# Performance work log

Measured on AMD Instinct MI355X. Metric: run time of the kernel, lower is better.

The kernel has to match this reference:

```python
import jax, jax.numpy as jnp
import numpy as np

N = 100000      # nodes
E = 1600000     # edges
IN = 128        # input features
HID = 16        # hidden per head
HEADS = 4
OUT = 40        # output classes per head
NEG = 0.2       # leaky_relu slope (DGL default)
EPS = 1e-5      # BN eps


def setup_inputs() -> dict:
    key = jax.random.key(0)
    ks = jax.random.split(key, 24)
    rn = lambda k, s, sc=0.1: jax.random.normal(k, s, jnp.float32) * sc
    return {
        "feat": rn(ks[0], (N, IN), 1.0),
        "src": jax.random.randint(ks[1], (E,), 0, N, jnp.int32),
        "dst": jax.random.randint(ks[2], (E,), 0, N, jnp.int32),
        "W0": rn(ks[3], (IN, HEADS * HID)),
        "al0": rn(ks[4], (HEADS, HID)),
        "ar0": rn(ks[5], (HEADS, HID)),
        "b0": jnp.zeros((HEADS * HID,), jnp.float32),
        "resW0": rn(ks[6], (IN, HEADS * HID)),
        "gamma0": jnp.ones((HEADS * HID,), jnp.float32),
        "beta0": jnp.zeros((HEADS * HID,), jnp.float32),
        "W1": rn(ks[7], (HEADS * HID, HEADS * HID)),
        "al1": rn(ks[8], (HEADS, HID)),
        "ar1": rn(ks[9], (HEADS, HID)),
        "b1": jnp.zeros((HEADS * HID,), jnp.float32),
        "gamma1": jnp.ones((HEADS * HID,), jnp.float32),
        "beta1": jnp.zeros((HEADS * HID,), jnp.float32),
        "W2": rn(ks[10], (HEADS * HID, HEADS * OUT)),
        "al2": rn(ks[11], (HEADS, OUT)),
        "ar2": rn(ks[12], (HEADS, OUT)),
        "b2": jnp.zeros((HEADS * OUT,), jnp.float32),
        "resW2": rn(ks[13], (HEADS * HID, HEADS * OUT)),
    }


def gat_conv(h, src, dst, W, al, ar, b, res):
    # h: [N, F_in]; res: [N, H*D] (res_fc output or identity)
    n = h.shape[0]
    H, D = al.shape
    feat = (h @ W).reshape(n, H, D)                 # [N,H,D]
    el = jnp.einsum('nhd,hd->nh', feat, al)         # [N,H]
    er = jnp.einsum('nhd,hd->nh', feat, ar)
    e = jax.nn.leaky_relu(el[src] + er[dst], NEG)   # [E,H]
    # edge softmax over destination nodes
    m = jax.ops.segment_max(e, dst, num_segments=n)
    ee = jnp.exp(e - m[dst])
    denom = jax.ops.segment_sum(ee, dst, num_segments=n)
    alpha = ee / jnp.maximum(denom[dst], 1e-16)     # [E,H]
    rst = jax.ops.segment_sum(alpha[:, :, None] * feat[src], dst, num_segments=n)
    rst = rst + res.reshape(n, H, D) + b.reshape(1, H, D)
    return rst.reshape(n, H * D)


def batch_norm(h, gamma, beta):
    mu = jnp.mean(h, axis=0)
    var = jnp.var(h, axis=0)
    return (h - mu) * jax.lax.rsqrt(var + EPS) * gamma + beta


def reference(feat, src, dst, W0, al0, ar0, b0, resW0, gamma0, beta0,
              W1, al1, ar1, b1, gamma1, beta1, W2, al2, ar2, b2, resW2):
    # layer 0: res_fc is a Linear (128 != 64); outer residual skipped (dims differ)
    h = gat_conv(feat, src, dst, W0, al0, ar0, b0, feat @ resW0)
    h = jax.nn.relu(batch_norm(h, gamma0, beta0))
    # layer 1: res_fc Identity (64 == 64); outer residual applies
    h1 = gat_conv(h, src, dst, W1, al1, ar1, b1, h)
    h1 = h1 + h
    h1 = jax.nn.relu(batch_norm(h1, gamma1, beta1))
    # layer 2 (output): res_fc Linear (64 != 160); no BN/ReLU, no outer residual
    out = gat_conv(h1, src, dst, W2, al2, ar2, b2, h1 @ resW2)
    return out
```

## Files before the change

kernel.cpp:

```cpp
#include <hip/hip_runtime.h>
#include <cstdint>

#define N_NODES 100000
#define N_EDGES 1600000
#define F_IN 128
#define HID 16
#define HEADS 4
#define OUTC 40
#define NEG_SLOPE 0.2f
#define BN_EPS 1e-5f

#define SCAN_B 256
#define SCAN_NB ((N_NODES + SCAN_B - 1) / SCAN_B)

static inline int cdiv(int a, int b){ return (a + b - 1) / b; }

__device__ __forceinline__ float bf2f(unsigned short u){
  union { unsigned u32; float f; } v; v.u32 = ((unsigned)u) << 16; return v.f;
}
__device__ __forceinline__ unsigned short f2bf(float x){
  union { float f; unsigned u; } v; v.f = x;
  unsigned r = v.u + 0x7FFFu + ((v.u >> 16) & 1u);
  return (unsigned short)(r >> 16);
}

__global__ void fill_f32(float* p, float v, int n){
  int i = blockIdx.x * blockDim.x + threadIdx.x;
  if (i < n) p[i] = v;
}
__global__ void fill_i32(int* p, int v, int n){
  int i = blockIdx.x * blockDim.x + threadIdx.x;
  if (i < n) p[i] = v;
}

template<int K, int M, int RT, bool BF16OUT>
__global__ __launch_bounds__((M / 4) * RT) void gemm_tiled(
    const float* __restrict__ A, const float* __restrict__ W,
    const float* __restrict__ bias, void* __restrict__ Cv, int n)
{
  constexpr int CT = M / 4;
  constexpr int BT = CT * RT;
  constexpr int ROWS = 64;
  constexpr int RPT = ROWS / RT;
  constexpr int KP = K + 4;
  __shared__ float ash[ROWS * KP];
  __shared__ float wsh[K * M];

  const int t = threadIdx.x;
  const int row0 = blockIdx.x * ROWS;

  const float4* Wv = (const float4*)W;
  for (int q = t; q < K * M / 4; q += BT)
    *(float4*)&wsh[q * 4] = Wv[q];

  for (int q = t; q < ROWS * K / 4; q += BT){
    int r = q / (K / 4);
    int kq = q - r * (K / 4);
    int grow = row0 + r;
    float4 v = make_float4(0.f, 0.f, 0.f, 0.f);
    if (grow < n) v = *(const float4*)&A[grow * K + kq * 4];
    *(float4*)&ash[r * KP + kq * 4] = v;
  }
  __syncthreads();

  const int c = t % CT;
  const int rt = t / CT;
  const int r0 = rt * RPT;

  float4 bb = make_float4(0.f, 0.f, 0.f, 0.f);
  if (bias) bb = ((const float4*)bias)[c];
  float4 acc[RPT];
  #pragma unroll
  for (int r = 0; r < RPT; ++r) acc[r] = bb;

  for (int k0 = 0; k0 < K; k0 += 4){
    float4 w0 = *(const float4*)&wsh[(k0 + 0) * M + c * 4];
    float4 w1 = *(const float4*)&wsh[(k0 + 1) * M + c * 4];
    float4 w2 = *(const float4*)&wsh[(k0 + 2) * M + c * 4];
    float4 w3 = *(const float4*)&wsh[(k0 + 3) * M + c * 4];
    #pragma unroll
    for (int r = 0; r < RPT; ++r){
      float4 a = *(const float4*)&ash[(r0 + r) * KP + k0];
      acc[r].x += a.x * w0.x + a.y * w1.x + a.z * w2.x + a.w * w3.x;
      acc[r].y += a.x * w0.y + a.y * w1.y + a.z * w2.y + a.w * w3.y;
      acc[r].z += a.x * w0.z + a.y * w1.z + a.z * w2.z + a.w * w3.z;
      acc[r].w += a.x * w0.w + a.y * w1.w + a.z * w2.w + a.w * w3.w;
    }
  }

  #pragma unroll
  for (int r = 0; r < RPT; ++r){
    int row = row0 + r0 + r;
    if (row < n){
      if (BF16OUT){
        ushort4 o;
        o.x = f2bf(acc[r].x); o.y = f2bf(acc[r].y);
        o.z = f2bf(acc[r].z); o.w = f2bf(acc[r].w);
        *(ushort4*)&((unsigned short*)Cv)[row * M + c * 4] = o;
      } else {
        *(float4*)&((float*)Cv)[row * M + c * 4] = acc[r];
      }
    }
  }
}

__global__ void elr_kernel(const unsigned short* __restrict__ featl,
                           const float* __restrict__ al, const float* __restrict__ ar,
                           float* __restrict__ el, float* __restrict__ er,
                           int n, int D){
  int idx = blockIdx.x * blockDim.x + threadIdx.x;
  if (idx >= n * HEADS) return;
  int h = idx & (HEADS - 1);
  const unsigned short* f = featl + (idx >> 2) * (HEADS * D) + h * D;
  float sl = 0.f, sr = 0.f;
  for (int d = 0; d < D; ++d){
    float v = bf2f(f[d]);
    sl += v * al[h * D + d];
    sr += v * ar[h * D + d];
  }
  el[idx] = sl;
  er[idx] = sr;
}

__global__ void residual2_kernel(float* __restrict__ hh, const float* __restrict__ b, int n, int F){
  int idx = blockIdx.x * blockDim.x + threadIdx.x;
  if (idx >= n * F) return;
  int f = idx % F;
  hh[idx] = 2.f * hh[idx] + b[f];
}

__global__ void hist_kernel(const int* __restrict__ dst, int* __restrict__ deg){
  int i = blockIdx.x * blockDim.x + threadIdx.x;
  if (i < N_EDGES) atomicAdd(&deg[dst[i]], 1);
}

__global__ __launch_bounds__(SCAN_B) void scan_partials(const int* __restrict__ deg,
                                                        int* __restrict__ part){
  __shared__ int s[SCAN_B];
  int t = threadIdx.x;
  int i = blockIdx.x * SCAN_B + t;
  s[t] = (i < N_NODES) ? deg[i] : 0;
  __syncthreads();
  #pragma unroll
  for (int off = SCAN_B / 2; off; off >>= 1){
    if (t < off) s[t] += s[t + off];
    __syncthreads();
  }
  if (t == 0) part[blockIdx.x] = s[0];
}

__global__ __launch_bounds__(512) void scan_offsets(int* __restrict__ part){
  __shared__ int s[512];
  int t = threadIdx.x;
  int v = (t < SCAN_NB) ? part[t] : 0;
  s[t] = v;
  __syncthreads();
  for (int off = 1; off < 512; off <<= 1){
    int u = (t >= off) ? s[t - off] : 0;
    __syncthreads();
    s[t] += u;
    __syncthreads();
  }
  if (t < SCAN_NB) part[t] = s[t] - v;
}

__global__ __launch_bounds__(SCAN_B) void scan_apply(const int* __restrict__ deg,
                                                     const int* __restrict__ part,
                                                     int* __restrict__ rowptr,
                                                     int* __restrict__ cursor){
  __shared__ int s[SCAN_B];
  int t = threadIdx.x;
  int i = blockIdx.x * SCAN_B + t;
  int v = (i < N_NODES) ? deg[i] : 0;
  s[t] = v;
  __syncthreads();
  for (int off = 1; off < SCAN_B; off <<= 1){
    int u = (t >= off) ? s[t - off] : 0;
    __syncthreads();
    s[t] += u;
    __syncthreads();
  }
  if (i < N_NODES){
    int ex = part[blockIdx.x] + s[t] - v;
    rowptr[i] = ex;
    cursor[i] = ex;
  }
  if (i == 0) rowptr[N_NODES] = N_EDGES;
}

__global__ void scatter_kernel(const int* __restrict__ src, const int* __restrict__ dst,
                               int* __restrict__ cursor, int* __restrict__ csr_src){
  int i = blockIdx.x * blockDim.x + threadIdx.x;
  if (i >= N_EDGES) return;
  int d = dst[i];
  int pos = atomicAdd(&cursor[d], 1);
  csr_src[pos] = src[i];
}

__device__ __forceinline__ float leaky(float x){ return x >= 0.f ? x : NEG_SLOPE * x; }
__device__ __forceinline__ float sel4(float4 v, int h){
  float r = v.x;
  r = (h == 1) ? v.y : r;
  r = (h == 2) ? v.z : r;
  r = (h == 3) ? v.w : r;
  return r;
}

template<int D>
__global__ __launch_bounds__(256) void node_agg_kernel(
    const int* __restrict__ rowptr, const int* __restrict__ csr_src,
    const float* __restrict__ el, const float* __restrict__ er,
    const unsigned short* __restrict__ featl, float* __restrict__ io)
{
  constexpr int F = HEADS * D;
  __shared__ float alds[4][64][4];
  __shared__ int   slds[4][64];
  int wid = threadIdx.x >> 6;
  int lane = threadIdx.x & 63;
  int node = blockIdx.x * 4 + wid;
  if (node >= N_NODES) return;
  int start = rowptr[node], end = rowptr[node + 1];
  int cnt = end - start;
  float4 erd = *(const float4*)(er + 4 * node);
  bool fast = (cnt <= 64);

  float4 mh, ih;
  if (fast){
    int sidx = 0;
    float x0 = -1e30f, x1 = -1e30f, x2 = -1e30f, x3 = -1e30f;
    if (lane < cnt){
      sidx = csr_src[start + lane];
      float4 e4 = *(const float4*)(el + 4 * sidx);
      x0 = leaky(e4.x + erd.x); x1 = leaky(e4.y + erd.y);
      x2 = leaky(e4.z + erd.z); x3 = leaky(e4.w + erd.w);
    }
    float m0 = x0, m1 = x1, m2 = x2, m3 = x3;
    #pragma unroll
    for (int off = 32; off; off >>= 1){
      m0 = fmaxf(m0, __shfl_xor(m0, off, 64));
      m1 = fmaxf(m1, __shfl_xor(m1, off, 64));
      m2 = fmaxf(m2, __shfl_xor(m2, off, 64));
      m3 = fmaxf(m3, __shfl_xor(m3, off, 64));
    }
    float e0 = 0.f, e1 = 0.f, e2 = 0.f, e3 = 0.f;
    if (lane < cnt){
      e0 = __expf(x0 - m0); e1 = __expf(x1 - m1);
      e2 = __expf(x2 - m2); e3 = __expf(x3 - m3);
    }
    float s0 = e0, s1 = e1, s2 = e2, s3 = e3;
    #pragma unroll
    for (int off = 32; off; off >>= 1){
      s0 += __shfl_xor(s0, off, 64);
      s1 += __shfl_xor(s1, off, 64);
      s2 += __shfl_xor(s2, off, 64);
      s3 += __shfl_xor(s3, off, 64);
    }
    ih = make_float4(1.f / fmaxf(s0, 1e-16f), 1.f / fmaxf(s1, 1e-16f),
                     1.f / fmaxf(s2, 1e-16f), 1.f / fmaxf(s3, 1e-16f));
    if (lane < cnt){
      slds[wid][lane] = sidx;
      float4 av = make_float4(e0 * ih.x, e1 * ih.y, e2 * ih.z, e3 * ih.w);
      *(float4*)&alds[wid][lane][0] = av;
    }
  } else {
    float m0 = -1e30f, m1 = -1e30f, m2 = -1e30f, m3 = -1e30f;
    for (int i = start + lane; i < end; i += 64){
      int s = csr_src[i];
      float4 e4 = *(const float4*)(el + 4 * s);
      m0 = fmaxf(m0, leaky(e4.x + erd.x));
      m1 = fmaxf(m1, leaky(e4.y + erd.y));
      m2 = fmaxf(m2, leaky(e4.z + erd.z));
      m3 = fmaxf(m3, leaky(e4.w + erd.w));
    }
    #pragma unroll
    for (int off = 32; off; off >>= 1){
      m0 = fmaxf(m0, __shfl_xor(m0, off, 64));
      m1 = fmaxf(m1, __shfl_xor(m1, off, 64));
      m2 = fmaxf(m2, __shfl_xor(m2, off, 64));
      m3 = fmaxf(m3, __shfl_xor(m3, off, 64));
    }
    float s0 = 0.f, s1 = 0.f, s2 = 0.f, s3 = 0.f;
    for (int i = start + lane; i < end; i += 64){
      int s = csr_src[i];
      float4 e4 = *(const float4*)(el + 4 * s);
      s0 += __expf(leaky(e4.x + erd.x) - m0);
      s1 += __expf(leaky(e4.y + erd.y) - m1);
      s2 += __expf(leaky(e4.z + erd.z) - m2);
      s3 += __expf(leaky(e4.w + erd.w) - m3);
    }
    #pragma unroll
    for (int off = 32; off; off >>= 1){
      s0 += __shfl_xor(s0, off, 64);
      s1 += __shfl_xor(s1, off, 64);
      s2 += __shfl_xor(s2, off, 64);
      s3 += __shfl_xor(s3, off, 64);
    }
    mh = make_float4(m0, m1, m2, m3);
    ih = make_float4(1.f / fmaxf(s0, 1e-16f), 1.f / fmaxf(s1, 1e-16f),
                     1.f / fmaxf(s2, 1e-16f), 1.f / fmaxf(s3, 1e-16f));
  }

  const int f0 = lane;
  const int h0 = f0 / D;
  float acc0 = io[node * F + f0];
  const unsigned short* fb = featl + f0;

  if (D == 16){
    if (fast){
      const float* ap = &alds[wid][0][h0];
      const int* sp = &slds[wid][0];
      int j = 0;
      for (; j + 3 < cnt; j += 4){
        int sA = sp[j], sB = sp[j + 1], sC = sp[j + 2], sD = sp[j + 3];
        float aA = ap[4 * j], aB = ap[4 * (j + 1)], aC = ap[4 * (j + 2)], aD = ap[4 * (j + 3)];
        acc0 += aA * bf2f(fb[sA * F]);
        acc0 += aB * bf2f(fb[sB * F]);
        acc0 += aC * bf2f(fb[sC * F]);
        acc0 += aD * bf2f(fb[sD * F]);
      }
      for (; j < cnt; ++j)
        acc0 += ap[4 * j] * bf2f(fb[sp[j] * F]);
    } else {
      const float er0 = sel4(erd, h0), mm0 = sel4(mh, h0), ii0 = sel4(ih, h0);
      for (int i = start; i < end; ++i){
        int s = csr_src[i];
        float4 e4 = *(const float4*)(el + 4 * s);
        acc0 += __expf(leaky(sel4(e4, h0) + er0) - mm0) * ii0 * bf2f(fb[s * F]);
      }
    }
    io[node * F + f0] = acc0;
  } else {
    const int h1 = (lane + 64) / D;
    const int h2 = 3;
    float acc1 = io[node * F + lane + 64];
    float acc2 = (lane < F - 128) ? io[node * F + lane + 128] : 0.f;
    if (fast){
      const float* ab = &alds[wid][0][0];
      const int* sp = &slds[wid][0];
      int j = 0;
      for (; j + 1 < cnt; j += 2){
        int sA = sp[j], sB = sp[j + 1];
        float aA0 = ab[4 * j + h0], aA1 = ab[4 * j + h1], aA2 = ab[4 * j + h2];
        float aB0 = ab[4 * (j + 1) + h0], aB1 = ab[4 * (j + 1) + h1], aB2 = ab[4 * (j + 1) + h2];
        acc0 += aA0 * bf2f(fb[sA * F]);
        acc1 += aA1 * bf2f(fb[sA * F + 64]);
        acc0 += aB0 * bf2f(fb[sB * F]);
        acc1 += aB1 * bf2f(fb[sB * F + 64]);
        if (lane < F - 128){
          acc2 += aA2 * bf2f(fb[sA * F + 128]);
          acc2 += aB2 * bf2f(fb[sB * F + 128]);
        }
      }
      for (; j < cnt; ++j){
        int s = sp[j];
        acc0 += ab[4 * j + h0] * bf2f(fb[s * F]);
        acc1 += ab[4 * j + h1] * bf2f(fb[s * F + 64]);
        if (lane < F - 128) acc2 += ab[4 * j + h2] * bf2f(fb[s * F + 128]);
      }
    } else {
      const float er0 = sel4(erd, h0), mm0 = sel4(mh, h0), ii0 = sel4(ih, h0);
      const float er1 = sel4(erd, h1), mm1 = sel4(mh, h1), ii1 = sel4(ih, h1);
      const float er2 = sel4(erd, h2), mm2 = sel4(mh, h2), ii2 = sel4(ih, h2);
      for (int i = start; i < end; ++i){
        int s = csr_src[i];
        float4 e4 = *(const float4*)(el + 4 * s);
        acc0 += __expf(leaky(sel4(e4, h0) + er0) - mm0) * ii0 * bf2f(fb[s * F]);
        acc1 += __expf(leaky(sel4(e4, h1) + er1) - mm1) * ii1 * bf2f(fb[s * F + 64]);
        if (lane < F - 128)
          acc2 += __expf(leaky(sel4(e4, h2) + er2) - mm2) * ii2 * bf2f(fb[s * F + 128]);
      }
    }
    io[node * F + f0] = acc0;
    io[node * F + lane + 64] = acc1;
    if (lane < F - 128) io[node * F + lane + 128] = acc2;
  }
}

__global__ void bn_stats_kernel(const float* __restrict__ x, float* __restrict__ sums, int n){
  __shared__ float s[512];
  int tid = threadIdx.x;
  int f = tid & 63, g = tid >> 6;
  float sm = 0.f, sq = 0.f;
  for (int r = blockIdx.x * 4 + g; r < n; r += gridDim.x * 4){
    float v = x[r * 64 + f];
    sm += v; sq += v * v;
  }
  s[tid] = sm; s[256 + tid] = sq;
  __syncthreads();
  if (g == 0){
    float a = s[f] + s[64 + f] + s[128 + f] + s[192 + f];
    float b = s[256 + f] + s[320 + f] + s[384 + f] + s[448 + f];
    atomicAdd(&sums[f], a);
    atomicAdd(&sums[64 + f], b);
  }
}

__global__ void bn_finalize_kernel(float* __restrict__ stats, int n){
  int f = threadIdx.x;
  if (f < 64){
    float mu = stats[f] / n;
    float var = stats[64 + f] / n - mu * mu;
    stats[128 + f] = mu;
    stats[192 + f] = rsqrtf(var + BN_EPS);
  }
}

__global__ void bn_apply_kernel(float* __restrict__ x, const float* __restrict__ stats,
                                const float* __restrict__ gamma, const float* __restrict__ beta,
                                int n){
  int idx = blockIdx.x * blockDim.x + threadIdx.x;
  if (idx >= n * 64) return;
  int f = idx & 63;
  float v = (x[idx] - stats[128 + f]) * stats[192 + f] * gamma[f] + beta[f];
  x[idx] = v > 0.f ? v : 0.f;
}

extern "C" void kernel_launch(void* const* d_in, const int* in_sizes, int n_in,
                              void* d_out, int out_size, void* d_ws, size_t ws_size,
                              hipStream_t stream){
  const float* feat  = (const float*)d_in[0];
  const int*   src   = (const int*)d_in[1];
  const int*   dst   = (const int*)d_in[2];
  const float* W0    = (const float*)d_in[3];
  const float* al0   = (const float*)d_in[4];
  const float* ar0   = (const float*)d_in[5];
  const float* b0    = (const float*)d_in[6];
  const float* resW0 = (const float*)d_in[7];
  const float* g0    = (const float*)d_in[8];
  const float* be0   = (const float*)d_in[9];
  const float* W1    = (const float*)d_in[10];
  const float* al1   = (const float*)d_in[11];
  const float* ar1   = (const float*)d_in[12];
  const float* b1    = (const float*)d_in[13];
  const float* g1    = (const float*)d_in[14];
  const float* be1   = (const float*)d_in[15];
  const float* W2    = (const float*)d_in[16];
  const float* al2   = (const float*)d_in[17];
  const float* ar2   = (const float*)d_in[18];
  const float* b2    = (const float*)d_in[19];
  const float* resW2 = (const float*)d_in[20];
  float* out = (float*)d_out;

  unsigned short* featl = (unsigned short*)d_ws;
  float* h     = (float*)(featl + N_NODES * 160);
  float* el    = h + N_NODES * 64;
  float* er    = el + N_NODES * 4;
  float* stats = er + N_NODES * 4;
  int* rowptr  = (int*)(stats + 256);
  int* cursor  = rowptr + (N_NODES + 1);
  int* deg     = cursor + N_NODES;
  int* part    = deg + N_NODES;
  int* csr_src = part + SCAN_NB + 1;

  const int B = 256;
  const int gNH  = cdiv(N_NODES * HEADS, B);
  const int gE   = cdiv(N_EDGES, B);
  const int g64  = cdiv(N_NODES * 64, B);
  const int gN   = cdiv(N_NODES, B);
  const int gAgg = cdiv(N_NODES, 4);
  const int gGemm = cdiv(N_NODES, 64);

  fill_i32<<<gN, B, 0, stream>>>(deg, 0, N_NODES);
  hist_kernel<<<gE, B, 0, stream>>>(dst, deg);
  scan_partials<<<SCAN_NB, SCAN_B, 0, stream>>>(deg, part);
  scan_offsets<<<1, 512, 0, stream>>>(part);
  scan_apply<<<SCAN_NB, SCAN_B, 0, stream>>>(deg, part, rowptr, cursor);
  scatter_kernel<<<gE, B, 0, stream>>>(src, dst, cursor, csr_src);

  gemm_tiled<128, 64, 16, true><<<gGemm, 256, 0, stream>>>(feat, W0, nullptr, featl, N_NODES);
  elr_kernel<<<gNH, B, 0, stream>>>(featl, al0, ar0, el, er, N_NODES, HID);
  gemm_tiled<128, 64, 16, false><<<gGemm, 256, 0, stream>>>(feat, resW0, b0, h, N_NODES);
  node_agg_kernel<HID><<<gAgg, 256, 0, stream>>>(rowptr, csr_src, el, er, featl, h);
  fill_f32<<<1, 128, 0, stream>>>(stats, 0.f, 128);
  bn_stats_kernel<<<512, 256, 0, stream>>>(h, stats, N_NODES);
  bn_finalize_kernel<<<1, 64, 0, stream>>>(stats, N_NODES);
  bn_apply_kernel<<<g64, B, 0, stream>>>(h, stats, g0, be0, N_NODES);

  gemm_tiled<64, 64, 16, true><<<gGemm, 256, 0, stream>>>(h, W1, nullptr, featl, N_NODES);
  elr_kernel<<<gNH, B, 0, stream>>>(featl, al1, ar1, el, er, N_NODES, HID);
  residual2_kernel<<<g64, B, 0, stream>>>(h, b1, N_NODES, 64);
  node_agg_kernel<HID><<<gAgg, 256, 0, stream>>>(rowptr, csr_src, el, er, featl, h);
  fill_f32<<<1, 128, 0, stream>>>(stats, 0.f, 128);
  bn_stats_kernel<<<512, 256, 0, stream>>>(h, stats, N_NODES);
  bn_finalize_kernel<<<1, 64, 0, stream>>>(stats, N_NODES);
  bn_apply_kernel<<<g64, B, 0, stream>>>(h, stats, g1, be1, N_NODES);

  gemm_tiled<64, 160, 8, true><<<gGemm, 320, 0, stream>>>(h, W2, nullptr, featl, N_NODES);
  elr_kernel<<<gNH, B, 0, stream>>>(featl, al2, ar2, el, er, N_NODES, OUTC);
  gemm_tiled<64, 160, 8, false><<<gGemm, 320, 0, stream>>>(h, resW2, b2, out, N_NODES);
  node_agg_kernel<OUTC><<<gAgg, 256, 0, stream>>>(rowptr, csr_src, el, er, featl, out);
}
```

Baseline: 1.002 ms.

## Build CSR via two-level bucket sort instead of global atomic scatter

```diff
diff --git a/kernel.cpp b/kernel.cpp
--- a/kernel.cpp
+++ b/kernel.cpp
@@ -10,8 +10,8 @@
 #define NEG_SLOPE 0.2f
 #define BN_EPS 1e-5f
 
-#define SCAN_B 256
-#define SCAN_NB ((N_NODES + SCAN_B - 1) / SCAN_B)
+#define NBUCK ((N_NODES + 127) / 128)
+#define SC_EDGES 16384
 
 static inline int cdiv(int a, int b){ return (a + b - 1) / b; }
 
@@ -129,72 +129,98 @@
   hh[idx] = 2.f * hh[idx] + b[f];
 }
 
-__global__ void hist_kernel(const int* __restrict__ dst, int* __restrict__ deg){
-  int i = blockIdx.x * blockDim.x + threadIdx.x;
-  if (i < N_EDGES) atomicAdd(&deg[dst[i]], 1);
-}
-
-__global__ __launch_bounds__(SCAN_B) void scan_partials(const int* __restrict__ deg,
-                                                        int* __restrict__ part){
-  __shared__ int s[SCAN_B];
+__global__ __launch_bounds__(256) void bucket_count(const int* __restrict__ dst,
+                                                    int* __restrict__ gcount){
+  __shared__ int lc[NBUCK];
   int t = threadIdx.x;
-  int i = blockIdx.x * SCAN_B + t;
-  s[t] = (i < N_NODES) ? deg[i] : 0;
-  __syncthreads();
-  #pragma unroll
-  for (int off = SCAN_B / 2; off; off >>= 1){
-    if (t < off) s[t] += s[t + off];
-    __syncthreads();
-  }
-  if (t == 0) part[blockIdx.x] = s[0];
-}
-
-__global__ __launch_bounds__(512) void scan_offsets(int* __restrict__ part){
-  __shared__ int s[512];
+  for (int i = t; i < NBUCK; i += 256) lc[i] = 0;
+  __syncthreads();
+  for (int i = blockIdx.x * 256 + t; i < N_EDGES; i += gridDim.x * 256)
+    atomicAdd(&lc[dst[i] >> 7], 1);
+  __syncthreads();
+  for (int i = t; i < NBUCK; i += 256)
+    if (lc[i]) atomicAdd(&gcount[i], lc[i]);
+}
+
+__global__ __launch_bounds__(1024) void bucket_scan(const int* __restrict__ gcount,
+                                                    int* __restrict__ bbase,
+                                                    int* __restrict__ gcursor){
+  __shared__ int s[1024];
   int t = threadIdx.x;
-  int v = (t < SCAN_NB) ? part[t] : 0;
+  int v = (t < NBUCK) ? gcount[t] : 0;
   s[t] = v;
   __syncthreads();
-  for (int off = 1; off < 512; off <<= 1){
+  for (int off = 1; off < 1024; off <<= 1){
     int u = (t >= off) ? s[t - off] : 0;
     __syncthreads();
     s[t] += u;
     __syncthreads();
   }
-  if (t < SCAN_NB) part[t] = s[t] - v;
-}
-
-__global__ __launch_bounds__(SCAN_B) void scan_apply(const int* __restrict__ deg,
-                                                     const int* __restrict__ part,
-                                                     int* __restrict__ rowptr,
-                                                     int* __restrict__ cursor){
-  __shared__ int s[SCAN_B];
+  if (t < NBUCK){ bbase[t] = s[t] - v; gcursor[t] = s[t] - v; }
+  if (t == NBUCK - 1) bbase[NBUCK] = s[t];
+}
+
+__global__ __launch_bounds__(256) void bucket_scatter(const int* __restrict__ src,
+                                                      const int* __restrict__ dst,
+                                                      int* __restrict__ gcursor,
+                                                      int2* __restrict__ pairs){
+  __shared__ int lc[NBUCK];
+  __shared__ int lp[NBUCK];
   int t = threadIdx.x;
-  int i = blockIdx.x * SCAN_B + t;
-  int v = (i < N_NODES) ? deg[i] : 0;
-  s[t] = v;
-  __syncthreads();
-  for (int off = 1; off < SCAN_B; off <<= 1){
-    int u = (t >= off) ? s[t - off] : 0;
+  int e0 = blockIdx.x * SC_EDGES;
+  int e1 = min(e0 + SC_EDGES, N_EDGES);
+  for (int i = t; i < NBUCK; i += 256) lc[i] = 0;
+  __syncthreads();
+  for (int i = e0 + t; i < e1; i += 256)
+    atomicAdd(&lc[dst[i] >> 7], 1);
+  __syncthreads();
+  for (int i = t; i < NBUCK; i += 256){
+    int c = lc[i];
+    lp[i] = c ? atomicAdd(&gcursor[i], c) : 0;
+  }
+  __syncthreads();
+  for (int i = e0 + t; i < e1; i += 256){
+    int d = dst[i];
+    int pos = atomicAdd(&lp[d >> 7], 1);
+    pairs[pos] = make_int2(src[i], d);
+  }
+}
+
+__global__ __launch_bounds__(256) void bucket_build(const int2* __restrict__ pairs,
+                                                    const int* __restrict__ bbase,
+                                                    int* __restrict__ rowptr,
+                                                    int* __restrict__ csr_src){
+  __shared__ int lh[128];
+  __shared__ int ls[128];
+  int b = blockIdx.x;
+  int t = threadIdx.x;
+  int s0 = bbase[b], s1 = bbase[b + 1];
+  if (t < 128) lh[t] = 0;
+  __syncthreads();
+  for (int i = s0 + t; i < s1; i += 256)
+    atomicAdd(&lh[pairs[i].y & 127], 1);
+  __syncthreads();
+  if (t < 128) ls[t] = lh[t];
+  __syncthreads();
+  for (int off = 1; off < 128; off <<= 1){
+    int u = (t < 128 && t >= off) ? ls[t - off] : 0;
     __syncthreads();
-    s[t] += u;
+    if (t < 128) ls[t] += u;
     __syncthreads();
   }
-  if (i < N_NODES){
-    int ex = part[blockIdx.x] + s[t] - v;
-    rowptr[i] = ex;
-    cursor[i] = ex;
-  }
-  if (i == 0) rowptr[N_NODES] = N_EDGES;
-}
-
-__global__ void scatter_kernel(const int* __restrict__ src, const int* __restrict__ dst,
-                               int* __restrict__ cursor, int* __restrict__ csr_src){
-  int i = blockIdx.x * blockDim.x + threadIdx.x;
-  if (i >= N_EDGES) return;
-  int d = dst[i];
-  int pos = atomicAdd(&cursor[d], 1);
-  csr_src[pos] = src[i];
+  if (t < 128){
+    int ex = s0 + ls[t] - lh[t];
+    int node = (b << 7) + t;
+    if (node < N_NODES) rowptr[node] = ex;
+    lh[t] = ex;
+  }
+  if (b == NBUCK - 1 && t == 0) rowptr[N_NODES] = N_EDGES;
+  __syncthreads();
+  for (int i = s0 + t; i < s1; i += 256){
+    int2 p = pairs[i];
+    int pos = atomicAdd(&lh[p.y & 127], 1);
+    csr_src[pos] = p.x;
+  }
 }
 
 __device__ __forceinline__ float leaky(float x){ return x >= 0.f ? x : NEG_SLOPE * x; }
@@ -441,31 +467,29 @@
   const float* resW2 = (const float*)d_in[20];
   float* out = (float*)d_out;
 
-  unsigned short* featl = (unsigned short*)d_ws;
+  int2* pairs  = (int2*)d_ws;
+  unsigned short* featl = (unsigned short*)(pairs + N_EDGES);
   float* h     = (float*)(featl + N_NODES * 160);
   float* el    = h + N_NODES * 64;
   float* er    = el + N_NODES * 4;
   float* stats = er + N_NODES * 4;
   int* rowptr  = (int*)(stats + 256);
-  int* cursor  = rowptr + (N_NODES + 1);
-  int* deg     = cursor + N_NODES;
-  int* part    = deg + N_NODES;
-  int* csr_src = part + SCAN_NB + 1;
+  int* gcount  = rowptr + (N_NODES + 1);
+  int* bbase   = gcount + NBUCK;
+  int* gcursor = bbase + NBUCK + 1;
+  int* csr_src = gcursor + NBUCK;
 
   const int B = 256;
   const int gNH  = cdiv(N_NODES * HEADS, B);
-  const int gE   = cdiv(N_EDGES, B);
   const int g64  = cdiv(N_NODES * 64, B);
-  const int gN   = cdiv(N_NODES, B);
   const int gAgg = cdiv(N_NODES, 4);
   const int gGemm = cdiv(N_NODES, 64);
 
-  fill_i32<<<gN, B, 0, stream>>>(deg, 0, N_NODES);
-  hist_kernel<<<gE, B, 0, stream>>>(dst, deg);
-  scan_partials<<<SCAN_NB, SCAN_B, 0, stream>>>(deg, part);
-  scan_offsets<<<1, 512, 0, stream>>>(part);
-  scan_apply<<<SCAN_NB, SCAN_B, 0, stream>>>(deg, part, rowptr, cursor);
-  scatter_kernel<<<gE, B, 0, stream>>>(src, dst, cursor, csr_src);
+  fill_i32<<<cdiv(NBUCK, B), B, 0, stream>>>(gcount, 0, NBUCK);
+  bucket_count<<<256, B, 0, stream>>>(dst, gcount);
+  bucket_scan<<<1, 1024, 0, stream>>>(gcount, bbase, gcursor);
+  bucket_scatter<<<cdiv(N_EDGES, SC_EDGES), B, 0, stream>>>(src, dst, gcursor, pairs);
+  bucket_build<<<NBUCK, B, 0, stream>>>(pairs, bbase, rowptr, csr_src);
 
   gemm_tiled<128, 64, 16, true><<<gGemm, 256, 0, stream>>>(feat, W0, nullptr, featl, N_NODES);
   elr_kernel<<<gNH, B, 0, stream>>>(featl, al0, ar0, el, er, N_NODES, HID);
```

New measurement: 915.5 us. 1.1x faster.
